# Kernel tuning notes

Measured on AMD Instinct MI355X. Metric: run time of the kernel, lower is better.

## Reference

```python
import jax, jax.numpy as jnp
import numpy as np

B = 12288
C = 1000


def setup_inputs() -> dict:
    key = jax.random.key(0)
    k1, k2 = jax.random.split(key)
    pred = jax.random.normal(k1, (B, C), dtype=jnp.float32)
    target = jax.random.randint(k2, (B,), 0, C)
    return {"pred": pred, "target": target, "num_classes": C}


def reference(pred, target, num_classes):
    # Vectorized form of the per-class loop: for a pair (b=negative, a=positive),
    # only class i = target[a] contributes, provided target[b] != target[a].
    #   margin[b, a] = pred[a, target[a]] - pred[b, target[a]]
    #   weight[b, a] = 1 / (N[target[b]] * N[target[a]])
    # loss = sum(hinge(margin) * weight) / (E * (E - 1)), E = #classes with N>0.
    N = jnp.zeros((num_classes,), jnp.float32).at[target].add(1.0)  # per-class counts
    E = jnp.sum(N > 0).astype(jnp.float32)  # exist_class_num
    f_own = jnp.take_along_axis(pred, target[:, None], axis=1)[:, 0]  # [B] pred[a, t[a]]
    P = pred[:, target]                      # [B, B]; P[b, a] = pred[b, target[a]]
    margin = f_own[None, :] - P              # [B_neg, B_pos]
    Nt = N[target]                            # [B] N[t[.]] (>= 1 always)
    diff = target[:, None] != target[None, :]  # t[b] != t[a]
    w = jnp.where(diff, 1.0 / (Nt[:, None] * Nt[None, :]), 0.0)
    loss = jnp.sum(jnp.maximum(1.0 - margin, 0.0) * w) / (E * (E - 1.0))
    return loss.reshape(1)
```

## Files before the change

### kernel.cpp

```cpp
#include <hip/hip_runtime.h>
#include <float.h>


#define CCLS 1000
#define PADF 64
#define TPB 256
#define CCH 250
#define NCH 4
#define NRBLK 512
#define RMAX 32

__global__ void k_init(int* fill) {
    int t = blockIdx.x * 256 + threadIdx.x;
    if (t < CCLS) fill[t] = 0;
}

__global__ void k_scatter(const float* __restrict__ pred, const int* __restrict__ target,
                          int* fill, float* thrP, int B) {
    int j = blockIdx.x * 256 + threadIdx.x;
    if (j >= B) return;
    int tj = target[j];
    float fo = pred[(size_t)j * CCLS + tj];
    int pos = atomicAdd(&fill[tj], 1);
    if (pos < PADF) thrP[tj * PADF + pos] = fo - 1.0f;
}

__global__ __launch_bounds__(256) void k_diag(const int* __restrict__ fill,
                                              float* thrP, float* invN, float* diagArr) {
    int c = (blockIdx.x * 256 + threadIdx.x) >> 6;
    int lane = threadIdx.x & 63;
    if (c >= CCLS) return;
    int cnt = fill[c];
    int cl = min(cnt, PADF);
    float v = (lane < cl) ? thrP[c * PADF + lane] : FLT_MAX;
    if (lane >= cl && lane < 32) thrP[c * PADF + lane] = FLT_MAX;
    float vp1 = v + 1.0f;
    float F = 0.f;
    for (int k = 0; k < cl; ++k) {
        float u = __shfl(v, k);
        F += fmaxf(vp1 - u, 0.f);
    }
    if (lane >= cl) F = 0.f;
    for (int o = 32; o; o >>= 1) F += __shfl_down(F, o);
    if (lane == 0) {
        if (cnt > 0) {
            float ic = 1.0f / (float)cnt;
            invN[c] = ic;
            diagArr[c] = F * ic * ic;
        } else {
            invN[c] = 0.f;
            diagArr[c] = 0.f;
        }
    }
}

#define BODYQ(NQ)                                                                   \
    {                                                                               \
        float4 tq[NQ];                                                              \
        _Pragma("unroll") for (int q = 0; q < NQ; ++q) tq[q] = tp4[q];              \
        const float fS = (float)(4 * NQ);                                           \
        int r = 0;                                                                  \
        _Pragma("unroll 1") for (; r + 8 <= rows; r += 8) {                         \
            const float p0 = pp[(size_t)(r + 0) * CCLS];                            \
            const float p1 = pp[(size_t)(r + 1) * CCLS];                            \
            const float p2 = pp[(size_t)(r + 2) * CCLS];                            \
            const float p3 = pp[(size_t)(r + 3) * CCLS];                            \
            const float p4 = pp[(size_t)(r + 4) * CCLS];                            \
            const float p5 = pp[(size_t)(r + 5) * CCLS];                            \
            const float p6 = pp[(size_t)(r + 6) * CCLS];                            \
            const float p7 = pp[(size_t)(r + 7) * CCLS];                            \
            float a0 = 0.f, a1 = 0.f, a2 = 0.f, a3 = 0.f;                           \
            float a4 = 0.f, a5 = 0.f, a6 = 0.f, a7 = 0.f;                           \
            _Pragma("unroll") for (int q = 0; q < NQ; ++q) {                        \
                a0 += (fminf(p0, tq[q].x) + fminf(p0, tq[q].y))                     \
                    + (fminf(p0, tq[q].z) + fminf(p0, tq[q].w));                    \
                a1 += (fminf(p1, tq[q].x) + fminf(p1, tq[q].y))                     \
                    + (fminf(p1, tq[q].z) + fminf(p1, tq[q].w));                    \
                a2 += (fminf(p2, tq[q].x) + fminf(p2, tq[q].y))                     \
                    + (fminf(p2, tq[q].z) + fminf(p2, tq[q].w));                    \
                a3 += (fminf(p3, tq[q].x) + fminf(p3, tq[q].y))                     \
                    + (fminf(p3, tq[q].z) + fminf(p3, tq[q].w));                    \
                a4 += (fminf(p4, tq[q].x) + fminf(p4, tq[q].y))                     \
                    + (fminf(p4, tq[q].z) + fminf(p4, tq[q].w));                    \
                a5 += (fminf(p5, tq[q].x) + fminf(p5, tq[q].y))                     \
                    + (fminf(p5, tq[q].z) + fminf(p5, tq[q].w));                    \
                a6 += (fminf(p6, tq[q].x) + fminf(p6, tq[q].y))                     \
                    + (fminf(p6, tq[q].z) + fminf(p6, tq[q].w));                    \
                a7 += (fminf(p7, tq[q].x) + fminf(p7, tq[q].y))                     \
                    + (fminf(p7, tq[q].z) + fminf(p7, tq[q].w));                    \
            }                                                                       \
            acc = fmaf(fmaf(fS, p0, -a0), rowW[r + 0], acc);                        \
            acc = fmaf(fmaf(fS, p1, -a1), rowW[r + 1], acc);                        \
            acc = fmaf(fmaf(fS, p2, -a2), rowW[r + 2], acc);                        \
            acc = fmaf(fmaf(fS, p3, -a3), rowW[r + 3], acc);                        \
            acc = fmaf(fmaf(fS, p4, -a4), rowW[r + 4], acc);                        \
            acc = fmaf(fmaf(fS, p5, -a5), rowW[r + 5], acc);                        \
            acc = fmaf(fmaf(fS, p6, -a6), rowW[r + 6], acc);                        \
            acc = fmaf(fmaf(fS, p7, -a7), rowW[r + 7], acc);                        \
        }                                                                           \
        for (; r < rows; ++r) {                                                     \
            const float p = pp[(size_t)r * CCLS];                                   \
            float a = 0.f;                                                          \
            _Pragma("unroll") for (int q = 0; q < NQ; ++q) {                        \
                a += (fminf(p, tq[q].x) + fminf(p, tq[q].y))                        \
                   + (fminf(p, tq[q].z) + fminf(p, tq[q].w));                       \
            }                                                                       \
            acc = fmaf(fmaf(fS, p, -a), rowW[r], acc);                              \
        }                                                                           \
    }

__global__ __launch_bounds__(TPB) void k_main(const float* __restrict__ pred,
        const int* __restrict__ target, const float* __restrict__ thrP,
        const float* __restrict__ invN, const int* __restrict__ fill,
        float* __restrict__ part, int B, int RPB) {
    __shared__ float rowW[RMAX];
    __shared__ float redL[TPB / 64];

    const int tid = threadIdx.x;
    const int chunk = blockIdx.x / NRBLK;
    const int rblk = blockIdx.x % NRBLK;
    const int c0 = chunk * CCH;
    const int rbase = rblk * RPB;
    const int rows = min(min(RPB, B - rbase), RMAX);

    for (int r = tid; r < rows; r += TPB) rowW[r] = invN[target[rbase + r]];
    __syncthreads();

    const int ccS = min(tid, CCH - 1);
    const int c = c0 + ccS;
    const float invc = (tid < CCH) ? invN[c] : 0.f;

    const int cnt = min(fill[c], PADF);
    int wmx = cnt;
    for (int o = 32; o; o >>= 1) wmx = max(wmx, __shfl_xor(wmx, o));

    const float* tg = thrP + (size_t)c * PADF;
    const float4* tp4 = (const float4*)tg;
    const float* pp = pred + (size_t)rbase * CCLS + c;
    float acc = 0.f;

    if (wmx <= 32) {
        const int nq = (wmx + 3) >> 2;
        switch ((nq + 1) >> 1) {
            case 0:
            case 1: BODYQ(2) break;
            case 2: BODYQ(4) break;
            case 3: BODYQ(6) break;
            default: BODYQ(8) break;
        }
    } else {
        for (int r = 0; r < rows; ++r) {
            const float p = pp[(size_t)r * CCLS];
            float s = 0.f;
            for (int k = 0; k < cnt; ++k) s += fminf(p, tg[k]);
            acc = fmaf(fmaf((float)cnt, p, -s), rowW[r], acc);
        }
    }
    acc *= invc;

    for (int o = 32; o; o >>= 1) acc += __shfl_down(acc, o);
    if ((tid & 63) == 0) redL[tid >> 6] = acc;
    __syncthreads();
    if (tid == 0) {
        float ssum = 0.f;
#pragma unroll
        for (int k = 0; k < TPB / 64; ++k) ssum += redL[k];
        part[blockIdx.x] = ssum;
    }
}

__global__ __launch_bounds__(1024) void k_final(const float* __restrict__ part, int npart,
        const float* __restrict__ invN, const float* __restrict__ diagArr,
        float* __restrict__ out) {
    __shared__ float wP[16], wD[16];
    __shared__ int wE[16];
    int tid = threadIdx.x;
    float sp = 0.f;
    for (int i = tid; i < npart; i += 1024) sp += part[i];
    float sd = 0.f;
    int se = 0;
    for (int c = tid; c < CCLS; c += 1024) {
        sd += diagArr[c];
        se += (invN[c] > 0.f) ? 1 : 0;
    }
    for (int o = 32; o; o >>= 1) {
        sp += __shfl_down(sp, o);
        sd += __shfl_down(sd, o);
        se += __shfl_down(se, o);
    }
    if ((tid & 63) == 0) { wP[tid >> 6] = sp; wD[tid >> 6] = sd; wE[tid >> 6] = se; }
    __syncthreads();
    if (tid == 0) {
        float tp = 0.f, td = 0.f;
        int te = 0;
#pragma unroll
        for (int k = 0; k < 16; ++k) { tp += wP[k]; td += wD[k]; te += wE[k]; }
        float E = (float)te;
        out[0] = (tp - td) / (E * (E - 1.0f));
    }
}

extern "C" void kernel_launch(void* const* d_in, const int* in_sizes, int n_in,
                              void* d_out, int out_size, void* d_ws, size_t ws_size,
                              hipStream_t stream) {
    const float* pred = (const float*)d_in[0];
    const int* target = (const int*)d_in[1];
    const int B = in_sizes[1];

    char* ws = (char*)d_ws;
    int* fill     = (int*)(ws + 0);
    float* invN   = (float*)(ws + 4096);
    float* diagAr = (float*)(ws + 8192);
    float* part   = (float*)(ws + 12288);
    float* thrP   = (float*)(ws + 24576);

    const int gb = (B + 255) / 256;
    const int RPB = (B + NRBLK - 1) / NRBLK;
    const int nblk = NCH * NRBLK;

    k_init<<<4, 256, 0, stream>>>(fill);
    k_scatter<<<gb, 256, 0, stream>>>(pred, target, fill, thrP, B);
    k_diag<<<(CCLS * 64 + 255) / 256, 256, 0, stream>>>(fill, thrP, invN, diagAr);
    k_main<<<nblk, TPB, 0, stream>>>(pred, target, thrP, invN, fill, part, B, RPB);
    k_final<<<1, 1024, 0, stream>>>(part, nblk, invN, diagAr, (float*)d_out);
}
```

Baseline: 44.02 us.

## Drop diag kernel, fold diagonal term into final reduction and inline inverse counts

Removes the separate k_diag launch. Threshold padding with FLT_MAX moves into the init kernel, inverse class counts are computed inline in the main kernel, and the per-class diagonal correction is computed inside the single-block final kernel using half-wave shuffles. It also switches pred indexing to 32-bit offsets and lowers the fast-path cutoff from 32 to 24 entries, dropping the NQ=8 specialization. The goal is to cut one launch and some intermediate traffic. The trade-off is serial diagonal work in one block, and any wave holding a class with more than 24 samples now takes the slow generic loop.

New measurement: 136.2 us. 3.09x slower.

```diff
diff --git a/kernel.cpp b/kernel.cpp
--- a/kernel.cpp
+++ b/kernel.cpp
@@ -8,11 +8,16 @@
 #define CCH 250
 #define NCH 4
 #define NRBLK 512
+#define NBLK (NCH * NRBLK)
 #define RMAX 32
 
-__global__ void k_init(int* fill) {
+__global__ void k_init(int* fill, float4* thrP4) {
     int t = blockIdx.x * 256 + threadIdx.x;
     if (t < CCLS) fill[t] = 0;
+    if (t < CCLS * 8) {
+        int c = t >> 3, q = t & 7;
+        thrP4[c * (PADF / 4) + q] = make_float4(FLT_MAX, FLT_MAX, FLT_MAX, FLT_MAX);
+    }
 }
 
 __global__ void k_scatter(const float* __restrict__ pred, const int* __restrict__ target,
@@ -25,35 +30,6 @@
     if (pos < PADF) thrP[tj * PADF + pos] = fo - 1.0f;
 }
 
-__global__ __launch_bounds__(256) void k_diag(const int* __restrict__ fill,
-                                              float* thrP, float* invN, float* diagArr) {
-    int c = (blockIdx.x * 256 + threadIdx.x) >> 6;
-    int lane = threadIdx.x & 63;
-    if (c >= CCLS) return;
-    int cnt = fill[c];
-    int cl = min(cnt, PADF);
-    float v = (lane < cl) ? thrP[c * PADF + lane] : FLT_MAX;
-    if (lane >= cl && lane < 32) thrP[c * PADF + lane] = FLT_MAX;
-    float vp1 = v + 1.0f;
-    float F = 0.f;
-    for (int k = 0; k < cl; ++k) {
-        float u = __shfl(v, k);
-        F += fmaxf(vp1 - u, 0.f);
-    }
-    if (lane >= cl) F = 0.f;
-    for (int o = 32; o; o >>= 1) F += __shfl_down(F, o);
-    if (lane == 0) {
-        if (cnt > 0) {
-            float ic = 1.0f / (float)cnt;
-            invN[c] = ic;
-            diagArr[c] = F * ic * ic;
-        } else {
-            invN[c] = 0.f;
-            diagArr[c] = 0.f;
-        }
-    }
-}
-
 #define BODYQ(NQ)                                                                   \
     {                                                                               \
         float4 tq[NQ];                                                              \
@@ -61,14 +37,15 @@
         const float fS = (float)(4 * NQ);                                           \
         int r = 0;                                                                  \
         _Pragma("unroll 1") for (; r + 8 <= rows; r += 8) {                         \
-            const float p0 = pp[(size_t)(r + 0) * CCLS];                            \
-            const float p1 = pp[(size_t)(r + 1) * CCLS];                            \
-            const float p2 = pp[(size_t)(r + 2) * CCLS];                            \
-            const float p3 = pp[(size_t)(r + 3) * CCLS];                            \
-            const float p4 = pp[(size_t)(r + 4) * CCLS];                            \
-            const float p5 = pp[(size_t)(r + 5) * CCLS];                            \
-            const float p6 = pp[(size_t)(r + 6) * CCLS];                            \
-            const float p7 = pp[(size_t)(r + 7) * CCLS];                            \
+            const int o = r * CCLS + c;                                             \
+            const float p0 = pb[o];                                                 \
+            const float p1 = pb[o + 1 * CCLS];                                      \
+            const float p2 = pb[o + 2 * CCLS];                                      \
+            const float p3 = pb[o + 3 * CCLS];                                      \
+            const float p4 = pb[o + 4 * CCLS];                                      \
+            const float p5 = pb[o + 5 * CCLS];                                      \
+            const float p6 = pb[o + 6 * CCLS];                                      \
+            const float p7 = pb[o + 7 * CCLS];                                      \
             float a0 = 0.f, a1 = 0.f, a2 = 0.f, a3 = 0.f;                           \
             float a4 = 0.f, a5 = 0.f, a6 = 0.f, a7 = 0.f;                           \
             _Pragma("unroll") for (int q = 0; q < NQ; ++q) {                        \
@@ -99,7 +76,7 @@
             acc = fmaf(fmaf(fS, p7, -a7), rowW[r + 7], acc);                        \
         }                                                                           \
         for (; r < rows; ++r) {                                                     \
-            const float p = pp[(size_t)r * CCLS];                                   \
+            const float p = pb[r * CCLS + c];                                       \
             float a = 0.f;                                                          \
             _Pragma("unroll") for (int q = 0; q < NQ; ++q) {                        \
                 a += (fminf(p, tq[q].x) + fminf(p, tq[q].y))                        \
@@ -111,7 +88,7 @@
 
 __global__ __launch_bounds__(TPB) void k_main(const float* __restrict__ pred,
         const int* __restrict__ target, const float* __restrict__ thrP,
-        const float* __restrict__ invN, const int* __restrict__ fill,
+        const int* __restrict__ fill,
         float* __restrict__ part, int B, int RPB) {
     __shared__ float rowW[RMAX];
     __shared__ float redL[TPB / 64];
@@ -123,34 +100,34 @@
     const int rbase = rblk * RPB;
     const int rows = min(min(RPB, B - rbase), RMAX);
 
-    for (int r = tid; r < rows; r += TPB) rowW[r] = invN[target[rbase + r]];
+    for (int r = tid; r < rows; r += TPB) {
+        int t = target[rbase + r];
+        rowW[r] = 1.0f / (float)fill[t];
+    }
     __syncthreads();
 
     const int ccS = min(tid, CCH - 1);
     const int c = c0 + ccS;
-    const float invc = (tid < CCH) ? invN[c] : 0.f;
-
-    const int cnt = min(fill[c], PADF);
+    const int cntR = fill[c];
+    const int cnt = min(cntR, PADF);
+    const float invc = (tid < CCH && cntR > 0) ? 1.0f / (float)cntR : 0.f;
+
     int wmx = cnt;
     for (int o = 32; o; o >>= 1) wmx = max(wmx, __shfl_xor(wmx, o));
 
-    const float* tg = thrP + (size_t)c * PADF;
-    const float4* tp4 = (const float4*)tg;
-    const float* pp = pred + (size_t)rbase * CCLS + c;
+    const float* pb = pred + (size_t)rbase * CCLS;
+    const float4* tp4 = (const float4*)(thrP + (size_t)c * PADF);
     float acc = 0.f;
 
-    if (wmx <= 32) {
+    if (wmx <= 24) {
         const int nq = (wmx + 3) >> 2;
-        switch ((nq + 1) >> 1) {
-            case 0:
-            case 1: BODYQ(2) break;
-            case 2: BODYQ(4) break;
-            case 3: BODYQ(6) break;
-            default: BODYQ(8) break;
-        }
+        if (nq <= 2)      { BODYQ(2) }
+        else if (nq <= 4) { BODYQ(4) }
+        else              { BODYQ(6) }
     } else {
+        const float* tg = thrP + (size_t)c * PADF;
         for (int r = 0; r < rows; ++r) {
-            const float p = pp[(size_t)r * CCLS];
+            const float p = pb[r * CCLS + c];
             float s = 0.f;
             for (int k = 0; k < cnt; ++k) s += fminf(p, tg[k]);
             acc = fmaf(fmaf((float)cnt, p, -s), rowW[r], acc);
@@ -169,32 +146,70 @@
     }
 }
 
-__global__ __launch_bounds__(1024) void k_final(const float* __restrict__ part, int npart,
-        const float* __restrict__ invN, const float* __restrict__ diagArr,
+__global__ __launch_bounds__(1024) void k_fin(const float* __restrict__ part,
+        const int* __restrict__ fill, const float* __restrict__ thrP,
         float* __restrict__ out) {
-    __shared__ float wP[16], wD[16];
+    __shared__ float wS[16], wD[16];
     __shared__ int wE[16];
-    int tid = threadIdx.x;
-    float sp = 0.f;
-    for (int i = tid; i < npart; i += 1024) sp += part[i];
-    float sd = 0.f;
-    int se = 0;
-    for (int c = tid; c < CCLS; c += 1024) {
-        sd += diagArr[c];
-        se += (invN[c] > 0.f) ? 1 : 0;
-    }
+    const int tid = threadIdx.x;
+    const int wid = tid >> 6, lane = tid & 63;
+    const int l2 = lane & 31;
+
+    float dsum = 0.f;
+    for (int cp = wid; cp < CCLS / 2; cp += 16) {
+        const int cA = 2 * cp, cB = 2 * cp + 1;
+        const int cntA = fill[cA], cntB = fill[cB];
+        if (cntA <= 31 && cntB <= 31) {
+            const int c = (lane >= 32) ? cB : cA;
+            const int cnt = (lane >= 32) ? cntB : cntA;
+            const float v = (l2 < cnt) ? thrP[(size_t)c * PADF + l2] : 0.f;
+            const float vp1 = v + 1.0f;
+            const int clmx = max(cntA, cntB);
+            float F = 0.f;
+            for (int k = 0; k < clmx; ++k) {
+                const float u = __shfl(v, k + (lane & 32));
+                F += (k < cnt) ? fmaxf(vp1 - u, 0.f) : 0.f;
+            }
+            if (l2 < cnt && cnt > 0) {
+                const float ic = 1.0f / (float)cnt;
+                dsum += F * ic * ic;
+            }
+        } else if (lane == 0) {
+            for (int s = 0; s < 2; ++s) {
+                const int c = s ? cB : cA;
+                const int cnt = fill[c];
+                const int cl = min(cnt, PADF);
+                if (cnt > 0) {
+                    float F = 0.f;
+                    for (int i = 0; i < cl; ++i) {
+                        const float fi = thrP[(size_t)c * PADF + i] + 1.0f;
+                        for (int k = 0; k < cl; ++k)
+                            F += fmaxf(fi - thrP[(size_t)c * PADF + k], 0.f);
+                    }
+                    const float ic = 1.0f / (float)cnt;
+                    dsum += F * ic * ic;
+                }
+            }
+        }
+    }
+
+    float psum = 0.f;
+    for (int i = tid; i < NBLK; i += 1024) psum += part[i];
+    int esum = 0;
+    for (int c = tid; c < CCLS; c += 1024) esum += (fill[c] > 0) ? 1 : 0;
+
     for (int o = 32; o; o >>= 1) {
-        sp += __shfl_down(sp, o);
-        sd += __shfl_down(sd, o);
-        se += __shfl_down(se, o);
-    }
-    if ((tid & 63) == 0) { wP[tid >> 6] = sp; wD[tid >> 6] = sd; wE[tid >> 6] = se; }
+        dsum += __shfl_down(dsum, o);
+        psum += __shfl_down(psum, o);
+        esum += __shfl_down(esum, o);
+    }
+    if (lane == 0) { wS[wid] = psum; wD[wid] = dsum; wE[wid] = esum; }
     __syncthreads();
     if (tid == 0) {
         float tp = 0.f, td = 0.f;
         int te = 0;
 #pragma unroll
-        for (int k = 0; k < 16; ++k) { tp += wP[k]; td += wD[k]; te += wE[k]; }
+        for (int k = 0; k < 16; ++k) { tp += wS[k]; td += wD[k]; te += wE[k]; }
         float E = (float)te;
         out[0] = (tp - td) / (E * (E - 1.0f));
     }
@@ -208,19 +223,15 @@
     const int B = in_sizes[1];
 
     char* ws = (char*)d_ws;
-    int* fill     = (int*)(ws + 0);
-    float* invN   = (float*)(ws + 4096);
-    float* diagAr = (float*)(ws + 8192);
-    float* part   = (float*)(ws + 12288);
-    float* thrP   = (float*)(ws + 24576);
+    int* fill   = (int*)(ws + 0);
+    float* part = (float*)(ws + 4096);
+    float* thrP = (float*)(ws + 16384);
 
     const int gb = (B + 255) / 256;
     const int RPB = (B + NRBLK - 1) / NRBLK;
-    const int nblk = NCH * NRBLK;
-
-    k_init<<<4, 256, 0, stream>>>(fill);
+
+    k_init<<<32, 256, 0, stream>>>(fill, (float4*)thrP);
     k_scatter<<<gb, 256, 0, stream>>>(pred, target, fill, thrP, B);
-    k_diag<<<(CCLS * 64 + 255) / 256, 256, 0, stream>>>(fill, thrP, invN, diagAr);
-    k_main<<<nblk, TPB, 0, stream>>>(pred, target, thrP, invN, fill, part, B, RPB);
-    k_final<<<1, 1024, 0, stream>>>(part, nblk, invN, diagAr, (float*)d_out);
-}
+    k_main<<<NBLK, TPB, 0, stream>>>(pred, target, thrP, fill, part, B, RPB);
+    k_fin<<<1, 1024, 0, stream>>>(part, fill, thrP, (float*)d_out);
+}
```
